# Kernel tuning notes

Measured on AMD Instinct MI355X. Metric: run time of the kernel, lower is better.

## Reference

```python
import jax, jax.numpy as jnp
import numpy as np
from jax import lax

B, C, H, W = 8, 128, 128, 128
HEADS = 16
HEAD_C = C // HEADS  # 8
SLOPE = 0.2
EPS = 1e-12


def _conv(x, w, b, padding, groups=1):
    # x: [B,C,H,W], w: [O,I/groups,kh,kw]
    y = lax.conv_general_dilated(
        x, w, window_strides=(1, 1), padding=padding,
        dimension_numbers=("NCHW", "OIHW", "NCHW"),
        feature_group_count=groups)
    return y + b[None, :, None, None]


def _conv_block(x, conv1_w, conv1_b, conv2_w, conv2_b, dw_w, dw_b, sc_w, sc_b):
    h = _conv(x, conv1_w, conv1_b, ((1, 1), (1, 1)))            # 3x3, zero pad
    h = jnp.where(h >= 0, h, SLOPE * h)                          # LeakyReLU
    h = _conv(h, conv2_w, conv2_b, ((0, 0), (0, 0)))             # 1x1
    hp = jnp.pad(h, ((0, 0), (0, 0), (1, 1), (1, 1)), mode="reflect")
    h = _conv(hp, dw_w, dw_b, ((0, 0), (0, 0)), groups=C)        # depthwise 3x3, reflect pad
    h = jnp.where(h >= 0, h, SLOPE * h)
    sc = _conv(x, sc_w, sc_b, ((0, 0), (0, 0)))                  # 1x1 shortcut
    return h + sc


def setup_inputs() -> dict:
    key = jax.random.key(0)
    ks = jax.random.split(key, 10)
    s = 0.05
    return {
        "x1": jax.random.normal(ks[0], (B, C, H, W), jnp.float32),
        "x2": jax.random.normal(ks[1], (B, C, H, W), jnp.float32),
        "temperature": jnp.ones((HEADS, 1, 1), jnp.float32),
        "conv1_w": jax.random.normal(ks[2], (C, C, 3, 3), jnp.float32) * s,
        "conv1_b": jnp.zeros((C,), jnp.float32),
        "conv2_w": jax.random.normal(ks[3], (C, C, 1, 1), jnp.float32) * s,
        "conv2_b": jnp.zeros((C,), jnp.float32),
        "dw_w": jax.random.normal(ks[4], (C, 1, 3, 3), jnp.float32) * s,
        "dw_b": jnp.zeros((C,), jnp.float32),
        "sc_w": jax.random.normal(ks[5], (C, C, 1, 1), jnp.float32) * s,
        "sc_b": jnp.zeros((C,), jnp.float32),
    }


def reference(x1, x2, temperature, conv1_w, conv1_b, conv2_w, conv2_b,
              dw_w, dw_b, sc_w, sc_b):
    b, c, h, w = x2.shape
    # b (head c) h w -> b head c (h w)
    qk = x1.reshape(b, HEADS, HEAD_C, h * w)
    v = x2.reshape(b, HEADS, HEAD_C, h * w)
    # L2-normalize over spatial dim (F.normalize, eps=1e-12)
    norm = jnp.sqrt(jnp.sum(qk * qk, axis=-1, keepdims=True))
    qn = qk / jnp.maximum(norm, EPS)
    # channel attention: [b, head, c, c]
    attn = jnp.einsum("bhcn,bhdn->bhcd", qn, qn) * temperature
    attn = jax.nn.softmax(attn, axis=-1)
    out = jnp.einsum("bhcd,bhdn->bhcn", attn, v)
    out = out.reshape(b, c, h, w)
    out = _conv_block(out, conv1_w, conv1_b, conv2_w, conv2_b,
                      dw_w, dw_b, sc_w, sc_b)
    return out + x1
```

## Files before the change

### kernel.cpp

```cpp
#include <hip/hip_runtime.h>
#include <hip/hip_bf16.h>

typedef __attribute__((ext_vector_type(8))) short short8;
typedef __attribute__((ext_vector_type(4))) float f32x4;

#define NB 8
#define NC 128
#define NHW 128
#define NSP (NHW*NHW)
#define SLOPE 0.2f
#define EPSN 1e-12f

static __device__ __forceinline__ unsigned short f2bf(float f) {
    __hip_bfloat16 h = __float2bfloat16(f);
    return *reinterpret_cast<unsigned short*>(&h);
}
static __device__ __forceinline__ float bf2f(__hip_bfloat16 h) {
    return __bfloat162float(h);
}

__global__ void prep_wb1(const float* __restrict__ w, __hip_bfloat16* __restrict__ wb) {
    int idx = blockIdx.x * 256 + threadIdx.x;
    if (idx >= 128 * 128 * 9) return;
    int kw = idx % 3; int t = idx / 3;
    int kh = t % 3;   t /= 3;
    int i  = t % 128; int o = t / 128;
    int tap = kh * 3 + kw;
    int q = i >> 5, lk = (i >> 3) & 3, j = i & 7;
    int wn = o >> 6, c = (o >> 4) & 3, l15 = o & 15;
    int lane = lk * 16 + l15;
    size_t chunk = ((size_t)(tap * 4 + q) * 2 + wn) * 4 + c;
    wb[chunk * 512 + lane * 8 + j] = __float2bfloat16(w[idx]);
}

__global__ void prep_w1x1(const float* __restrict__ w, __hip_bfloat16* __restrict__ wb) {
    int idx = blockIdx.x * 256 + threadIdx.x;
    if (idx >= 128 * 128) return;
    int i = idx & 127, o = idx >> 7;
    int kk = i >> 5, lk = (i >> 3) & 3, j = i & 7;
    int wn = o >> 6, c = (o >> 4) & 3, l15 = o & 15;
    int lane = lk * 16 + l15;
    size_t chunk = ((size_t)(wn * 4 + kk) * 4 + c);
    wb[chunk * 512 + lane * 8 + j] = __float2bfloat16(w[idx]);
}

__global__ __launch_bounds__(256) void gram_part(const float* __restrict__ x1,
                                                 float* __restrict__ Gp) {
    int bh = blockIdx.x & 127;
    int q  = blockIdx.x >> 7;
    const float* base = x1 + (size_t)bh * 8 * NSP + q * 4096;
    float acc[8][8];
#pragma unroll
    for (int c = 0; c < 8; c++)
#pragma unroll
        for (int d = 0; d < 8; d++) acc[c][d] = 0.f;

    for (int n = threadIdx.x; n < 4096; n += 256) {
        float v[8];
#pragma unroll
        for (int c = 0; c < 8; c++) v[c] = base[c * NSP + n];
#pragma unroll
        for (int c = 0; c < 8; c++)
#pragma unroll
            for (int d = 0; d < 8; d++)
                acc[c][d] = fmaf(v[c], v[d], acc[c][d]);
    }
#pragma unroll
    for (int c = 0; c < 8; c++)
#pragma unroll
        for (int d = 0; d < 8; d++)
            for (int off = 32; off > 0; off >>= 1)
                acc[c][d] += __shfl_down(acc[c][d], off);

    __shared__ float red[4][64];
    int wv = threadIdx.x >> 6;
    if ((threadIdx.x & 63) == 0) {
#pragma unroll
        for (int c = 0; c < 8; c++)
#pragma unroll
            for (int d = 0; d < 8; d++) red[wv][c * 8 + d] = acc[c][d];
    }
    __syncthreads();
    if (threadIdx.x < 64)
        Gp[(size_t)(q * 128 + bh) * 64 + threadIdx.x] =
            red[0][threadIdx.x] + red[1][threadIdx.x] + red[2][threadIdx.x] + red[3][threadIdx.x];
}

__global__ void gram_reduce(const float* __restrict__ Gp, float* __restrict__ G) {
    int bh = blockIdx.x;
    int t = threadIdx.x;
    float s = 0.f;
#pragma unroll
    for (int q = 0; q < 4; q++) s += Gp[(size_t)(q * 128 + bh) * 64 + t];
    G[bh * 64 + t] = s;
}

__global__ void softmax_kernel(const float* __restrict__ G, const float* __restrict__ temp,
                               float* __restrict__ attn) {
    int bh = blockIdx.x; int h = bh & 15;
    int t = threadIdx.x;
    int c = t >> 3, d = t & 7;
    const float* g = G + bh * 64;
    float nc = fmaxf(sqrtf(g[c * 8 + c]), EPSN);
    float nd = fmaxf(sqrtf(g[d * 8 + d]), EPSN);
    float a = g[t] / (nc * nd) * temp[h];
    float m = a;
#pragma unroll
    for (int off = 4; off > 0; off >>= 1) m = fmaxf(m, __shfl_xor(m, off));
    float e = __expf(a - m);
    float s = e;
#pragma unroll
    for (int off = 4; off > 0; off >>= 1) s += __shfl_xor(s, off);
    attn[bh * 64 + t] = e / s;
}

__global__ __launch_bounds__(256) void av_v2(const float* __restrict__ x2,
                                             const float* __restrict__ attn,
                                             __hip_bfloat16* __restrict__ yt) {
    int b  = blockIdx.x >> 8;
    int p0 = (blockIdx.x & 255) << 6;
    __shared__ float vt[128][65];
    __shared__ float at[16][65];
    for (int idx = threadIdx.x; idx < 1024; idx += 256)
        at[idx >> 6][idx & 63] = attn[(size_t)b * 1024 + idx];
    for (int idx = threadIdx.x; idx < 8192; idx += 256) {
        int row = idx >> 6, col = idx & 63;
        vt[row][col] = x2[(size_t)(b * 128 + row) * NSP + p0 + col];
    }
    __syncthreads();
    for (int idx = threadIdx.x; idx < 1024; idx += 256) {
        int cq = idx & 15;
        int p  = idx >> 4;
        float vv[8];
#pragma unroll
        for (int d = 0; d < 8; d++) vv[d] = vt[cq * 8 + d][p];
        unsigned int pk[4];
#pragma unroll
        for (int c = 0; c < 8; c += 2) {
            float s0 = 0.f, s1 = 0.f;
#pragma unroll
            for (int d = 0; d < 8; d++) {
                s0 = fmaf(at[cq][c * 8 + d], vv[d], s0);
                s1 = fmaf(at[cq][(c + 1) * 8 + d], vv[d], s1);
            }
            pk[c >> 1] = (unsigned int)f2bf(s0) | ((unsigned int)f2bf(s1) << 16);
        }
        uint4 st; st.x = pk[0]; st.y = pk[1]; st.z = pk[2]; st.w = pk[3];
        *reinterpret_cast<uint4*>(yt + ((size_t)b * NSP + p0 + p) * 128 + cq * 8) = st;
    }
}

__global__ __launch_bounds__(256, 3) void fused_conv(const __hip_bfloat16* __restrict__ yt,
                                                     const __hip_bfloat16* __restrict__ wb1,
                                                     const __hip_bfloat16* __restrict__ wb2,
                                                     const __hip_bfloat16* __restrict__ wbsc,
                                                     const float* __restrict__ b1,
                                                     const float* __restrict__ b2,
                                                     const float* __restrict__ bsc,
                                                     const float* __restrict__ x1,
                                                     __hip_bfloat16* __restrict__ h2,
                                                     float* __restrict__ out) {
    __shared__ uint4 smem[2048];
    char* smem_raw = (char*)smem;
    int bid = blockIdx.x;
    int blk = (bid & 7) * 128 + (bid >> 3);
    int b = blk >> 7, h = blk & 127;
    int tid = threadIdx.x;
    int lane = tid & 63;
    int wid = tid >> 6;
    int wm = wid >> 1, wn = wid & 1;
    int l15 = lane & 15;
    int lk = lane >> 4;

    const short8* wf1  = reinterpret_cast<const short8*>(wb1);
    const short8* wf2  = reinterpret_cast<const short8*>(wb2);
    const short8* wfsc = reinterpret_cast<const short8*>(wbsc);

    f32x4 acc[4][4];
#pragma unroll
    for (int a = 0; a < 4; a++)
#pragma unroll
        for (int c = 0; c < 4; c++) acc[a][c] = (f32x4){0.f, 0.f, 0.f, 0.f};

#pragma unroll
    for (int q = 0; q < 4; ++q) {
        __syncthreads();
        for (int idx = tid; idx < 1584; idx += 256) {
            int g = idx & 3;
            int colr = idx >> 2;
            int col = colr % 132;
            int r = colr / 132;
            int hh = h + r - 1;
            int w = col - 1;
            uint4 v = make_uint4(0u, 0u, 0u, 0u);
            if ((unsigned)hh < 128u && (unsigned)w < 128u)
                v = *reinterpret_cast<const uint4*>(
                    yt + (((size_t)(b * 128 + hh)) * 128 + w) * 128 + q * 32 + g * 8);
            smem[(r * 4 + g) * 132 + col] = v;
        }
        __syncthreads();

        const short8* wp0 = wf1 + ((size_t)((0 * 4 + q) * 2 + wn) * 4) * 64 + lane;
        short8 cb0 = wp0[0], cb1 = wp0[64], cb2 = wp0[128], cb3 = wp0[192];

#pragma unroll
        for (int tap = 0; tap < 9; ++tap) {
            int kh = tap / 3, kw = tap - kh * 3;
            short8 nb0, nb1, nb2, nb3;
            if (tap < 8) {
                const short8* wpn = wf1 + ((size_t)(((tap + 1) * 4 + q) * 2 + wn) * 4) * 64 + lane;
                nb0 = wpn[0]; nb1 = wpn[64]; nb2 = wpn[128]; nb3 = wpn[192];
            }
            short8 afr[4];
#pragma unroll
            for (int a = 0; a < 4; ++a) {
                int col = (wm * 4 + a) * 16 + l15 + kw;
                afr[a] = *reinterpret_cast<const short8*>(&smem[(kh * 4 + lk) * 132 + col]);
            }
            __builtin_amdgcn_s_setprio(1);
#pragma unroll
            for (int a = 0; a < 4; ++a) {
                acc[a][0] = __builtin_amdgcn_mfma_f32_16x16x32_bf16(afr[a], cb0, acc[a][0], 0, 0, 0);
                acc[a][1] = __builtin_amdgcn_mfma_f32_16x16x32_bf16(afr[a], cb1, acc[a][1], 0, 0, 0);
                acc[a][2] = __builtin_amdgcn_mfma_f32_16x16x32_bf16(afr[a], cb2, acc[a][2], 0, 0, 0);
                acc[a][3] = __builtin_amdgcn_mfma_f32_16x16x32_bf16(afr[a], cb3, acc[a][3], 0, 0, 0);
            }
            __builtin_amdgcn_s_setprio(0);
            if (tap < 8) { cb0 = nb0; cb1 = nb1; cb2 = nb2; cb3 = nb3; }
        }
    }

    __syncthreads();
#pragma unroll
    for (int c = 0; c < 4; ++c) {
        int o = wn * 64 + c * 16 + l15;
        float bv = b1[o];
        int go = o >> 3, ob = (o & 7) << 1;
#pragma unroll
        for (int a = 0; a < 4; ++a) {
            int pb = (wm * 4 + a) * 16 + lk * 4;
#pragma unroll
            for (int j = 0; j < 4; ++j) {
                int p = pb + j;
                float v = acc[a][c][j] + bv;
                v = v >= 0.f ? v : SLOPE * v;
                *reinterpret_cast<__hip_bfloat16*>(
                    smem_raw + p * 256 + (((go ^ (p & 15)) << 4) | ob)) = __float2bfloat16(v);
            }
        }
    }
    __syncthreads();

#pragma unroll
    for (int a = 0; a < 4; a++)
#pragma unroll
        for (int c = 0; c < 4; c++) acc[a][c] = (f32x4){0.f, 0.f, 0.f, 0.f};
#pragma unroll
    for (int kk = 0; kk < 4; ++kk) {
        short8 bfr[4];
#pragma unroll
        for (int c = 0; c < 4; ++c)
            bfr[c] = wf2[((size_t)(wn * 4 + kk) * 4 + c) * 64 + lane];
        short8 afr[4];
        int g = kk * 4 + lk;
#pragma unroll
        for (int a = 0; a < 4; ++a) {
            int p = (wm * 4 + a) * 16 + l15;
            afr[a] = *reinterpret_cast<const short8*>(smem_raw + p * 256 + ((g ^ (p & 15)) << 4));
        }
        __builtin_amdgcn_s_setprio(1);
#pragma unroll
        for (int a = 0; a < 4; ++a)
#pragma unroll
            for (int c = 0; c < 4; ++c)
                acc[a][c] = __builtin_amdgcn_mfma_f32_16x16x32_bf16(afr[a], bfr[c], acc[a][c], 0, 0, 0);
        __builtin_amdgcn_s_setprio(0);
    }
#pragma unroll
    for (int c = 0; c < 4; ++c) {
        int o = wn * 64 + c * 16 + l15;
        float bv = b2[o];
        size_t obase = ((size_t)(b * 128 + o) * 128 + h) * 128;
#pragma unroll
        for (int a = 0; a < 4; ++a) {
            int w0 = (wm * 4 + a) * 16 + lk * 4;
            uint2 st;
            st.x = (unsigned int)f2bf(acc[a][c][0] + bv) | ((unsigned int)f2bf(acc[a][c][1] + bv) << 16);
            st.y = (unsigned int)f2bf(acc[a][c][2] + bv) | ((unsigned int)f2bf(acc[a][c][3] + bv) << 16);
            *reinterpret_cast<uint2*>(h2 + obase + w0) = st;
        }
    }

    __syncthreads();
    for (int idx = tid; idx < 2048; idx += 256) {
        int p = idx >> 4, g = idx & 15;
        uint4 v = *reinterpret_cast<const uint4*>(
            yt + ((size_t)(b * NSP + h * 128 + p)) * 128 + g * 8);
        *reinterpret_cast<uint4*>(smem_raw + p * 256 + ((g ^ (p & 15)) << 4)) = v;
    }
    __syncthreads();

#pragma unroll
    for (int a = 0; a < 4; a++)
#pragma unroll
        for (int c = 0; c < 4; c++) acc[a][c] = (f32x4){0.f, 0.f, 0.f, 0.f};
#pragma unroll
    for (int kk = 0; kk < 4; ++kk) {
        short8 bfr[4];
#pragma unroll
        for (int c = 0; c < 4; ++c)
            bfr[c] = wfsc[((size_t)(wn * 4 + kk) * 4 + c) * 64 + lane];
        short8 afr[4];
        int g = kk * 4 + lk;
#pragma unroll
        for (int a = 0; a < 4; ++a) {
            int p = (wm * 4 + a) * 16 + l15;
            afr[a] = *reinterpret_cast<const short8*>(smem_raw + p * 256 + ((g ^ (p & 15)) << 4));
        }
        __builtin_amdgcn_s_setprio(1);
#pragma unroll
        for (int a = 0; a < 4; ++a)
#pragma unroll
            for (int c = 0; c < 4; ++c)
                acc[a][c] = __builtin_amdgcn_mfma_f32_16x16x32_bf16(afr[a], bfr[c], acc[a][c], 0, 0, 0);
        __builtin_amdgcn_s_setprio(0);
    }
#pragma unroll
    for (int c = 0; c < 4; ++c) {
        int o = wn * 64 + c * 16 + l15;
        float bv = bsc[o];
        size_t obase = ((size_t)(b * 128 + o) * 128 + h) * 128;
#pragma unroll
        for (int a = 0; a < 4; ++a) {
            int w0 = (wm * 4 + a) * 16 + lk * 4;
            float4 xv = *reinterpret_cast<const float4*>(x1 + obase + w0);
            float4 st;
            st.x = acc[a][c][0] + bv + xv.x;
            st.y = acc[a][c][1] + bv + xv.y;
            st.z = acc[a][c][2] + bv + xv.z;
            st.w = acc[a][c][3] + bv + xv.w;
            *reinterpret_cast<float4*>(out + obase + w0) = st;
        }
    }
}

__global__ __launch_bounds__(256) void dw_v2(const __hip_bfloat16* __restrict__ h2,
                                             const float* __restrict__ dww,
                                             const float* __restrict__ dwb,
                                             float* __restrict__ out) {
    int bid = blockIdx.x;
    int swz = (bid & 7) * 1024 + (bid >> 3);
    size_t tidx = (size_t)swz * 256 + threadIdx.x;
    int w0 = (int)((tidx & 15) << 3);
    int hh = (int)((tidx >> 4) & 127);
    int bc = (int)(tidx >> 11);
    int c  = bc & 127;
    const __hip_bfloat16* src = h2 + ((size_t)bc << 14);
    float wg[9];
#pragma unroll
    for (int k = 0; k < 9; ++k) wg[k] = dww[c * 9 + k];
    float bv = dwb[c];
    float a8[8];
#pragma unroll
    for (int j = 0; j < 8; ++j) a8[j] = bv;
#pragma unroll
    for (int kh = 0; kh < 3; ++kh) {
        int ih = hh + kh - 1;
        ih = ih < 0 ? 1 : (ih > 127 ? 126 : ih);
        const __hip_bfloat16* row = src + ih * 128;
        short8 mid = *reinterpret_cast<const short8*>(row + w0);
        float v[10];
        v[0] = bf2f(row[w0 == 0 ? 1 : w0 - 1]);
#pragma unroll
        for (int j = 0; j < 8; ++j)
            v[j + 1] = __uint_as_float((unsigned int)(unsigned short)mid[j] << 16);
        v[9] = bf2f(row[w0 == 120 ? 126 : w0 + 8]);
#pragma unroll
        for (int kw = 0; kw < 3; ++kw)
#pragma unroll
            for (int j = 0; j < 8; ++j)
                a8[j] = fmaf(v[j + kw], wg[kh * 3 + kw], a8[j]);
    }
    size_t ob = ((size_t)bc << 14) + hh * 128 + w0;
    float4 o0 = *reinterpret_cast<const float4*>(out + ob);
    float4 o1 = *reinterpret_cast<const float4*>(out + ob + 4);
#pragma unroll
    for (int j = 0; j < 8; ++j) a8[j] = a8[j] >= 0.f ? a8[j] : SLOPE * a8[j];
    o0.x += a8[0]; o0.y += a8[1]; o0.z += a8[2]; o0.w += a8[3];
    o1.x += a8[4]; o1.y += a8[5]; o1.z += a8[6]; o1.w += a8[7];
    *reinterpret_cast<float4*>(out + ob) = o0;
    *reinterpret_cast<float4*>(out + ob + 4) = o1;
}

extern "C" void kernel_launch(void* const* d_in, const int* in_sizes, int n_in,
                              void* d_out, int out_size, void* d_ws, size_t ws_size,
                              hipStream_t stream) {
    const float* x1   = (const float*)d_in[0];
    const float* x2   = (const float*)d_in[1];
    const float* temp = (const float*)d_in[2];
    const float* c1w  = (const float*)d_in[3];
    const float* c1b  = (const float*)d_in[4];
    const float* c2w  = (const float*)d_in[5];
    const float* c2b  = (const float*)d_in[6];
    const float* dww  = (const float*)d_in[7];
    const float* dwb  = (const float*)d_in[8];
    const float* scw  = (const float*)d_in[9];
    const float* scb  = (const float*)d_in[10];
    float* out = (float*)d_out;
    char* ws = (char*)d_ws;

    float*          G    = (float*)(ws);
    float*          attn = (float*)(ws + (32 << 10));
    float*          Gp   = (float*)(ws + (64 << 10));
    __hip_bfloat16* wb1  = (__hip_bfloat16*)(ws + (192 << 10));
    __hip_bfloat16* wb2  = (__hip_bfloat16*)(ws + (480 << 10));
    __hip_bfloat16* wbsc = (__hip_bfloat16*)(ws + (512 << 10));
    __hip_bfloat16* yt   = (__hip_bfloat16*)(ws + ((size_t)1 << 20));
    __hip_bfloat16* h2b  = (__hip_bfloat16*)(ws + ((size_t)34 << 20));

    prep_wb1<<<576, 256, 0, stream>>>(c1w, wb1);
    prep_w1x1<<<64, 256, 0, stream>>>(c2w, wb2);
    prep_w1x1<<<64, 256, 0, stream>>>(scw, wbsc);

    gram_part<<<512, 256, 0, stream>>>(x1, Gp);
    gram_reduce<<<128, 64, 0, stream>>>(Gp, G);
    softmax_kernel<<<128, 64, 0, stream>>>(G, temp, attn);
    av_v2<<<2048, 256, 0, stream>>>(x2, attn, yt);

    fused_conv<<<1024, 256, 0, stream>>>(yt, wb1, wb2, wbsc, c1b, c2b, scb, x1, h2b, out);
    dw_v2<<<8192, 256, 0, stream>>>(h2b, dww, dwb, out);
}
```

Before: 159.8 us.

## Split fused conv tiles to half rows with 64-channel K stages and swizzled LDS

The fused conv block now processes half an image row (64 pixels) per workgroup instead of a full row, which doubles the grid to 2048 blocks and halves the accumulators. The input halo is staged in two 64-channel halves with an XOR-swizzled LDS layout, and the 3x3 weights are re-laid out so each stage walks 18 tap/sub-chunk steps. Shared memory drops from 32 KB to about 25 KB and the occupancy hint rises to 4 blocks per CU, aiming for better latency hiding and load balance. In exchange the halo overhead grows (66 of 64 columns), and weight fragments are reloaded twice as often per output pixel.

```diff
diff --git a/kernel.cpp b/kernel.cpp
--- a/kernel.cpp
+++ b/kernel.cpp
@@ -26,10 +26,10 @@
     int kh = t % 3;   t /= 3;
     int i  = t % 128; int o = t / 128;
     int tap = kh * 3 + kw;
-    int q = i >> 5, lk = (i >> 3) & 3, j = i & 7;
+    int half = i >> 6, icc = (i >> 5) & 1, lk = (i >> 3) & 3, j = i & 7;
     int wn = o >> 6, c = (o >> 4) & 3, l15 = o & 15;
     int lane = lk * 16 + l15;
-    size_t chunk = ((size_t)(tap * 4 + q) * 2 + wn) * 4 + c;
+    size_t chunk = (size_t)tap * 32 + half * 16 + wn * 8 + icc * 4 + c;
     wb[chunk * 512 + lane * 8 + j] = __float2bfloat16(w[idx]);
 }
 
@@ -150,7 +150,7 @@
     }
 }
 
-__global__ __launch_bounds__(256, 3) void fused_conv(const __hip_bfloat16* __restrict__ yt,
+__global__ __launch_bounds__(256, 4) void fused_conv(const __hip_bfloat16* __restrict__ yt,
                                                      const __hip_bfloat16* __restrict__ wb1,
                                                      const __hip_bfloat16* __restrict__ wb2,
                                                      const __hip_bfloat16* __restrict__ wbsc,
@@ -160,11 +160,14 @@
                                                      const float* __restrict__ x1,
                                                      __hip_bfloat16* __restrict__ h2,
                                                      float* __restrict__ out) {
-    __shared__ uint4 smem[2048];
+    __shared__ uint4 smem[1584];
     char* smem_raw = (char*)smem;
     int bid = blockIdx.x;
-    int blk = (bid & 7) * 128 + (bid >> 3);
-    int b = blk >> 7, h = blk & 127;
+    int swz = (bid & 7) * 256 + (bid >> 3);
+    int b = swz >> 8;
+    int rh = swz & 255;
+    int h = rh >> 1;
+    int p0 = (rh & 1) * 64;
     int tid = threadIdx.x;
     int lane = tid & 63;
     int wid = tid >> 6;
@@ -176,57 +179,63 @@
     const short8* wf2  = reinterpret_cast<const short8*>(wb2);
     const short8* wfsc = reinterpret_cast<const short8*>(wbsc);
 
-    f32x4 acc[4][4];
-#pragma unroll
-    for (int a = 0; a < 4; a++)
+    f32x4 acc[2][4];
+#pragma unroll
+    for (int a = 0; a < 2; a++)
 #pragma unroll
         for (int c = 0; c < 4; c++) acc[a][c] = (f32x4){0.f, 0.f, 0.f, 0.f};
 
 #pragma unroll
-    for (int q = 0; q < 4; ++q) {
+    for (int half = 0; half < 2; ++half) {
         __syncthreads();
         for (int idx = tid; idx < 1584; idx += 256) {
-            int g = idx & 3;
-            int colr = idx >> 2;
-            int col = colr % 132;
-            int r = colr / 132;
+            int g = idx & 7;
+            int colr = idx >> 3;
+            int col = colr % 66;
+            int r = colr / 66;
             int hh = h + r - 1;
-            int w = col - 1;
+            int w = p0 + col - 1;
             uint4 v = make_uint4(0u, 0u, 0u, 0u);
             if ((unsigned)hh < 128u && (unsigned)w < 128u)
                 v = *reinterpret_cast<const uint4*>(
-                    yt + (((size_t)(b * 128 + hh)) * 128 + w) * 128 + q * 32 + g * 8);
-            smem[(r * 4 + g) * 132 + col] = v;
+                    yt + (((size_t)(b * 128 + hh)) * 128 + w) * 128 + half * 64 + g * 8);
+            smem[(r * 66 + col) * 8 + (g ^ (col & 7))] = v;
         }
         __syncthreads();
 
-        const short8* wp0 = wf1 + ((size_t)((0 * 4 + q) * 2 + wn) * 4) * 64 + lane;
+        int cgrp = half * 16 + wn * 8;
+        const short8* wp0 = wf1 + (size_t)cgrp * 64 + lane;
         short8 cb0 = wp0[0], cb1 = wp0[64], cb2 = wp0[128], cb3 = wp0[192];
 
 #pragma unroll
-        for (int tap = 0; tap < 9; ++tap) {
+        for (int gi = 0; gi < 18; ++gi) {
+            int tap = gi >> 1, icc = gi & 1;
             int kh = tap / 3, kw = tap - kh * 3;
             short8 nb0, nb1, nb2, nb3;
-            if (tap < 8) {
-                const short8* wpn = wf1 + ((size_t)(((tap + 1) * 4 + q) * 2 + wn) * 4) * 64 + lane;
+            if (gi < 17) {
+                int gin = gi + 1;
+                const short8* wpn = wf1 +
+                    (size_t)(((gin >> 1) * 32) + cgrp + (gin & 1) * 4) * 64 + lane;
                 nb0 = wpn[0]; nb1 = wpn[64]; nb2 = wpn[128]; nb3 = wpn[192];
             }
-            short8 afr[4];
-#pragma unroll
-            for (int a = 0; a < 4; ++a) {
-                int col = (wm * 4 + a) * 16 + l15 + kw;
-                afr[a] = *reinterpret_cast<const short8*>(&smem[(kh * 4 + lk) * 132 + col]);
+            short8 afr[2];
+#pragma unroll
+            for (int a = 0; a < 2; ++a) {
+                int col = (wm * 2 + a) * 16 + l15 + kw;
+                int g = icc * 4 + lk;
+                afr[a] = *reinterpret_cast<const short8*>(
+                    &smem[(kh * 66 + col) * 8 + (g ^ (col & 7))]);
             }
             __builtin_amdgcn_s_setprio(1);
 #pragma unroll
-            for (int a = 0; a < 4; ++a) {
+            for (int a = 0; a < 2; ++a) {
                 acc[a][0] = __builtin_amdgcn_mfma_f32_16x16x32_bf16(afr[a], cb0, acc[a][0], 0, 0, 0);
                 acc[a][1] = __builtin_amdgcn_mfma_f32_16x16x32_bf16(afr[a], cb1, acc[a][1], 0, 0, 0);
                 acc[a][2] = __builtin_amdgcn_mfma_f32_16x16x32_bf16(afr[a], cb2, acc[a][2], 0, 0, 0);
                 acc[a][3] = __builtin_amdgcn_mfma_f32_16x16x32_bf16(afr[a], cb3, acc[a][3], 0, 0, 0);
             }
             __builtin_amdgcn_s_setprio(0);
-            if (tap < 8) { cb0 = nb0; cb1 = nb1; cb2 = nb2; cb3 = nb3; }
+            cb0 = nb0; cb1 = nb1; cb2 = nb2; cb3 = nb3;
         }
     }
 
@@ -237,8 +246,8 @@
         float bv = b1[o];
         int go = o >> 3, ob = (o & 7) << 1;
 #pragma unroll
-        for (int a = 0; a < 4; ++a) {
-            int pb = (wm * 4 + a) * 16 + lk * 4;
+        for (int a = 0; a < 2; ++a) {
+            int pb = (wm * 2 + a) * 16 + lk * 4;
 #pragma unroll
             for (int j = 0; j < 4; ++j) {
                 int p = pb + j;
@@ -252,7 +261,7 @@
     __syncthreads();
 
 #pragma unroll
-    for (int a = 0; a < 4; a++)
+    for (int a = 0; a < 2; a++)
 #pragma unroll
         for (int c = 0; c < 4; c++) acc[a][c] = (f32x4){0.f, 0.f, 0.f, 0.f};
 #pragma unroll
@@ -261,16 +270,16 @@
 #pragma unroll
         for (int c = 0; c < 4; ++c)
             bfr[c] = wf2[((size_t)(wn * 4 + kk) * 4 + c) * 64 + lane];
-        short8 afr[4];
+        short8 afr[2];
         int g = kk * 4 + lk;
 #pragma unroll
-        for (int a = 0; a < 4; ++a) {
-            int p = (wm * 4 + a) * 16 + l15;
+        for (int a = 0; a < 2; ++a) {
+            int p = (wm * 2 + a) * 16 + l15;
             afr[a] = *reinterpret_cast<const short8*>(smem_raw + p * 256 + ((g ^ (p & 15)) << 4));
         }
         __builtin_amdgcn_s_setprio(1);
 #pragma unroll
-        for (int a = 0; a < 4; ++a)
+        for (int a = 0; a < 2; ++a)
 #pragma unroll
             for (int c = 0; c < 4; ++c)
                 acc[a][c] = __builtin_amdgcn_mfma_f32_16x16x32_bf16(afr[a], bfr[c], acc[a][c], 0, 0, 0);
@@ -280,10 +289,10 @@
     for (int c = 0; c < 4; ++c) {
         int o = wn * 64 + c * 16 + l15;
         float bv = b2[o];
-        size_t obase = ((size_t)(b * 128 + o) * 128 + h) * 128;
-#pragma unroll
-        for (int a = 0; a < 4; ++a) {
-            int w0 = (wm * 4 + a) * 16 + lk * 4;
+        size_t obase = ((size_t)(b * 128 + o) * 128 + h) * 128 + p0;
+#pragma unroll
+        for (int a = 0; a < 2; ++a) {
+            int w0 = (wm * 2 + a) * 16 + lk * 4;
             uint2 st;
             st.x = (unsigned int)f2bf(acc[a][c][0] + bv) | ((unsigned int)f2bf(acc[a][c][1] + bv) << 16);
             st.y = (unsigned int)f2bf(acc[a][c][2] + bv) | ((unsigned int)f2bf(acc[a][c][3] + bv) << 16);
@@ -292,16 +301,16 @@
     }
 
     __syncthreads();
-    for (int idx = tid; idx < 2048; idx += 256) {
+    for (int idx = tid; idx < 1024; idx += 256) {
         int p = idx >> 4, g = idx & 15;
         uint4 v = *reinterpret_cast<const uint4*>(
-            yt + ((size_t)(b * NSP + h * 128 + p)) * 128 + g * 8);
+            yt + ((size_t)(b * NSP + h * 128 + p0 + p)) * 128 + g * 8);
         *reinterpret_cast<uint4*>(smem_raw + p * 256 + ((g ^ (p & 15)) << 4)) = v;
     }
     __syncthreads();
 
 #pragma unroll
-    for (int a = 0; a < 4; a++)
+    for (int a = 0; a < 2; a++)
 #pragma unroll
         for (int c = 0; c < 4; c++) acc[a][c] = (f32x4){0.f, 0.f, 0.f, 0.f};
 #pragma unroll
@@ -310,16 +319,16 @@
 #pragma unroll
         for (int c = 0; c < 4; ++c)
             bfr[c] = wfsc[((size_t)(wn * 4 + kk) * 4 + c) * 64 + lane];
-        short8 afr[4];
+        short8 afr[2];
         int g = kk * 4 + lk;
 #pragma unroll
-        for (int a = 0; a < 4; ++a) {
-            int p = (wm * 4 + a) * 16 + l15;
+        for (int a = 0; a < 2; ++a) {
+            int p = (wm * 2 + a) * 16 + l15;
             afr[a] = *reinterpret_cast<const short8*>(smem_raw + p * 256 + ((g ^ (p & 15)) << 4));
         }
         __builtin_amdgcn_s_setprio(1);
 #pragma unroll
-        for (int a = 0; a < 4; ++a)
+        for (int a = 0; a < 2; ++a)
 #pragma unroll
             for (int c = 0; c < 4; ++c)
                 acc[a][c] = __builtin_amdgcn_mfma_f32_16x16x32_bf16(afr[a], bfr[c], acc[a][c], 0, 0, 0);
@@ -329,10 +338,10 @@
     for (int c = 0; c < 4; ++c) {
         int o = wn * 64 + c * 16 + l15;
         float bv = bsc[o];
-        size_t obase = ((size_t)(b * 128 + o) * 128 + h) * 128;
-#pragma unroll
-        for (int a = 0; a < 4; ++a) {
-            int w0 = (wm * 4 + a) * 16 + lk * 4;
+        size_t obase = ((size_t)(b * 128 + o) * 128 + h) * 128 + p0;
+#pragma unroll
+        for (int a = 0; a < 2; ++a) {
+            int w0 = (wm * 2 + a) * 16 + lk * 4;
             float4 xv = *reinterpret_cast<const float4*>(x1 + obase + w0);
             float4 st;
             st.x = acc[a][c][0] + bv + xv.x;
@@ -427,6 +436,6 @@
     softmax_kernel<<<128, 64, 0, stream>>>(G, temp, attn);
     av_v2<<<2048, 256, 0, stream>>>(x2, attn, yt);
 
-    fused_conv<<<1024, 256, 0, stream>>>(yt, wb1, wb2, wbsc, c1b, c2b, scb, x1, h2b, out);
+    fused_conv<<<2048, 256, 0, stream>>>(yt, wb1, wb2, wbsc, c1b, c2b, scb, x1, h2b, out);
     dw_v2<<<8192, 256, 0, stream>>>(h2b, dww, dwb, out);
 }
```

Result: no change. 162.4 us (+1.6%).

## Pad activations in global memory and load conv A-fragments directly, halve tile

Applied to the files above, without the earlier changes.

The attention output is now written into a zero-bordered 130x130 NHWC buffer, with a small kernel zeroing the border, so the 3x3 conv can read its A fragments straight from global memory with no bounds checks and no LDS staging. Each block now covers half an image row (64 pixels) with each wave owning 32 output channels, which halves LDS use and doubles the block count. Launch bounds are raised to 5 blocks per SM. This removes the staging barriers and LDS traffic of the conv1 stage, but relies on L1/L2 for the overlapping reads across taps.

```diff
diff --git a/kernel.cpp b/kernel.cpp
--- a/kernel.cpp
+++ b/kernel.cpp
@@ -10,6 +10,7 @@
 #define NSP (NHW*NHW)
 #define SLOPE 0.2f
 #define EPSN 1e-12f
+#define PADW 130
 
 static __device__ __forceinline__ unsigned short f2bf(float f) {
     __hip_bfloat16 h = __float2bfloat16(f);
@@ -26,10 +27,10 @@
     int kh = t % 3;   t /= 3;
     int i  = t % 128; int o = t / 128;
     int tap = kh * 3 + kw;
-    int q = i >> 5, lk = (i >> 3) & 3, j = i & 7;
-    int wn = o >> 6, c = (o >> 4) & 3, l15 = o & 15;
+    int g32 = i >> 5, lk = (i >> 3) & 3, j = i & 7;
+    int f = o >> 4, l15 = o & 15;
     int lane = lk * 16 + l15;
-    size_t chunk = ((size_t)(tap * 4 + q) * 2 + wn) * 4 + c;
+    size_t chunk = (size_t)(tap * 4 + g32) * 8 + f;
     wb[chunk * 512 + lane * 8 + j] = __float2bfloat16(w[idx]);
 }
 
@@ -38,10 +39,25 @@
     if (idx >= 128 * 128) return;
     int i = idx & 127, o = idx >> 7;
     int kk = i >> 5, lk = (i >> 3) & 3, j = i & 7;
-    int wn = o >> 6, c = (o >> 4) & 3, l15 = o & 15;
+    int f = o >> 4, l15 = o & 15;
     int lane = lk * 16 + l15;
-    size_t chunk = ((size_t)(wn * 4 + kk) * 4 + c);
+    size_t chunk = (size_t)kk * 8 + f;
     wb[chunk * 512 + lane * 8 + j] = __float2bfloat16(w[idx]);
+}
+
+__global__ void pad_zero(__hip_bfloat16* __restrict__ yt2) {
+    int t = blockIdx.x * 256 + threadIdx.x;
+    if (t >= 8 * 516) return;
+    int b = t / 516, s = t % 516;
+    int row, col;
+    if (s < 130)      { row = 0;           col = s; }
+    else if (s < 260) { row = 129;         col = s - 130; }
+    else if (s < 388) { row = s - 260 + 1; col = 0; }
+    else              { row = s - 388 + 1; col = 129; }
+    uint4* dst = reinterpret_cast<uint4*>(yt2 + ((size_t)(b * PADW + row) * PADW + col) * 128);
+    uint4 z = make_uint4(0u, 0u, 0u, 0u);
+#pragma unroll
+    for (int i = 0; i < 16; ++i) dst[i] = z;
 }
 
 __global__ __launch_bounds__(256) void gram_part(const float* __restrict__ x1,
@@ -114,9 +130,9 @@
     attn[bh * 64 + t] = e / s;
 }
 
-__global__ __launch_bounds__(256) void av_v2(const float* __restrict__ x2,
+__global__ __launch_bounds__(256) void av_v3(const float* __restrict__ x2,
                                              const float* __restrict__ attn,
-                                             __hip_bfloat16* __restrict__ yt) {
+                                             __hip_bfloat16* __restrict__ yt2) {
     int b  = blockIdx.x >> 8;
     int p0 = (blockIdx.x & 255) << 6;
     __shared__ float vt[128][65];
@@ -146,11 +162,14 @@
             pk[c >> 1] = (unsigned int)f2bf(s0) | ((unsigned int)f2bf(s1) << 16);
         }
         uint4 st; st.x = pk[0]; st.y = pk[1]; st.z = pk[2]; st.w = pk[3];
-        *reinterpret_cast<uint4*>(yt + ((size_t)b * NSP + p0 + p) * 128 + cq * 8) = st;
-    }
-}
-
-__global__ __launch_bounds__(256, 3) void fused_conv(const __hip_bfloat16* __restrict__ yt,
+        int n = p0 + p;
+        int hh = n >> 7, wc = n & 127;
+        *reinterpret_cast<uint4*>(
+            yt2 + ((size_t)(b * PADW + hh + 1) * PADW + wc + 1) * 128 + cq * 8) = st;
+    }
+}
+
+__global__ __launch_bounds__(256, 5) void fused_conv(const __hip_bfloat16* __restrict__ yt2,
                                                      const __hip_bfloat16* __restrict__ wb1,
                                                      const __hip_bfloat16* __restrict__ wb2,
                                                      const __hip_bfloat16* __restrict__ wbsc,
@@ -160,15 +179,17 @@
                                                      const float* __restrict__ x1,
                                                      __hip_bfloat16* __restrict__ h2,
                                                      float* __restrict__ out) {
-    __shared__ uint4 smem[2048];
+    __shared__ uint4 smem[1024];
     char* smem_raw = (char*)smem;
     int bid = blockIdx.x;
-    int blk = (bid & 7) * 128 + (bid >> 3);
-    int b = blk >> 7, h = blk & 127;
+    int swz = (bid & 7) * 256 + (bid >> 3);
+    int b = swz >> 8;
+    int rh = swz & 255;
+    int h = rh >> 1;
+    int p0 = (rh & 1) * 64;
     int tid = threadIdx.x;
     int lane = tid & 63;
     int wid = tid >> 6;
-    int wm = wid >> 1, wn = wid & 1;
     int l15 = lane & 15;
     int lk = lane >> 4;
 
@@ -176,73 +197,55 @@
     const short8* wf2  = reinterpret_cast<const short8*>(wb2);
     const short8* wfsc = reinterpret_cast<const short8*>(wbsc);
 
-    f32x4 acc[4][4];
-#pragma unroll
-    for (int a = 0; a < 4; a++)
-#pragma unroll
-        for (int c = 0; c < 4; c++) acc[a][c] = (f32x4){0.f, 0.f, 0.f, 0.f};
-
-#pragma unroll
-    for (int q = 0; q < 4; ++q) {
-        __syncthreads();
-        for (int idx = tid; idx < 1584; idx += 256) {
-            int g = idx & 3;
-            int colr = idx >> 2;
-            int col = colr % 132;
-            int r = colr / 132;
-            int hh = h + r - 1;
-            int w = col - 1;
-            uint4 v = make_uint4(0u, 0u, 0u, 0u);
-            if ((unsigned)hh < 128u && (unsigned)w < 128u)
-                v = *reinterpret_cast<const uint4*>(
-                    yt + (((size_t)(b * 128 + hh)) * 128 + w) * 128 + q * 32 + g * 8);
-            smem[(r * 4 + g) * 132 + col] = v;
-        }
-        __syncthreads();
-
-        const short8* wp0 = wf1 + ((size_t)((0 * 4 + q) * 2 + wn) * 4) * 64 + lane;
-        short8 cb0 = wp0[0], cb1 = wp0[64], cb2 = wp0[128], cb3 = wp0[192];
-
+    f32x4 acc[4][2];
+#pragma unroll
+    for (int m = 0; m < 4; m++) { acc[m][0] = (f32x4){0,0,0,0}; acc[m][1] = (f32x4){0,0,0,0}; }
+
+    const __hip_bfloat16* abase = yt2 + ((size_t)(b * PADW + h) * PADW + (p0 + l15)) * 128 + lk * 8;
+
+#pragma unroll
+    for (int g32 = 0; g32 < 4; ++g32) {
+        const short8* wp0 = wf1 + ((size_t)(0 * 4 + g32) * 8 + wid * 2) * 64 + lane;
+        short8 cb0 = wp0[0], cb1 = wp0[64];
 #pragma unroll
         for (int tap = 0; tap < 9; ++tap) {
             int kh = tap / 3, kw = tap - kh * 3;
-            short8 nb0, nb1, nb2, nb3;
+            short8 nb0, nb1;
             if (tap < 8) {
-                const short8* wpn = wf1 + ((size_t)(((tap + 1) * 4 + q) * 2 + wn) * 4) * 64 + lane;
-                nb0 = wpn[0]; nb1 = wpn[64]; nb2 = wpn[128]; nb3 = wpn[192];
+                const short8* wpn = wf1 + ((size_t)((tap + 1) * 4 + g32) * 8 + wid * 2) * 64 + lane;
+                nb0 = wpn[0]; nb1 = wpn[64];
             }
-            short8 afr[4];
-#pragma unroll
-            for (int a = 0; a < 4; ++a) {
-                int col = (wm * 4 + a) * 16 + l15 + kw;
-                afr[a] = *reinterpret_cast<const short8*>(&smem[(kh * 4 + lk) * 132 + col]);
-            }
+            const __hip_bfloat16* arow = abase + (size_t)(kh * PADW + kw) * 128 + g32 * 32;
+            short8 a0 = *reinterpret_cast<const short8*>(arow);
+            short8 a1 = *reinterpret_cast<const short8*>(arow + 2048);
+            short8 a2 = *reinterpret_cast<const short8*>(arow + 4096);
+            short8 a3 = *reinterpret_cast<const short8*>(arow + 6144);
             __builtin_amdgcn_s_setprio(1);
-#pragma unroll
-            for (int a = 0; a < 4; ++a) {
-                acc[a][0] = __builtin_amdgcn_mfma_f32_16x16x32_bf16(afr[a], cb0, acc[a][0], 0, 0, 0);
-                acc[a][1] = __builtin_amdgcn_mfma_f32_16x16x32_bf16(afr[a], cb1, acc[a][1], 0, 0, 0);
-                acc[a][2] = __builtin_amdgcn_mfma_f32_16x16x32_bf16(afr[a], cb2, acc[a][2], 0, 0, 0);
-                acc[a][3] = __builtin_amdgcn_mfma_f32_16x16x32_bf16(afr[a], cb3, acc[a][3], 0, 0, 0);
-            }
+            acc[0][0] = __builtin_amdgcn_mfma_f32_16x16x32_bf16(a0, cb0, acc[0][0], 0, 0, 0);
+            acc[0][1] = __builtin_amdgcn_mfma_f32_16x16x32_bf16(a0, cb1, acc[0][1], 0, 0, 0);
+            acc[1][0] = __builtin_amdgcn_mfma_f32_16x16x32_bf16(a1, cb0, acc[1][0], 0, 0, 0);
+            acc[1][1] = __builtin_amdgcn_mfma_f32_16x16x32_bf16(a1, cb1, acc[1][1], 0, 0, 0);
+            acc[2][0] = __builtin_amdgcn_mfma_f32_16x16x32_bf16(a2, cb0, acc[2][0], 0, 0, 0);
+            acc[2][1] = __builtin_amdgcn_mfma_f32_16x16x32_bf16(a2, cb1, acc[2][1], 0, 0, 0);
+            acc[3][0] = __builtin_amdgcn_mfma_f32_16x16x32_bf16(a3, cb0, acc[3][0], 0, 0, 0);
+            acc[3][1] = __builtin_amdgcn_mfma_f32_16x16x32_bf16(a3, cb1, acc[3][1], 0, 0, 0);
             __builtin_amdgcn_s_setprio(0);
-            if (tap < 8) { cb0 = nb0; cb1 = nb1; cb2 = nb2; cb3 = nb3; }
-        }
-    }
-
-    __syncthreads();
-#pragma unroll
-    for (int c = 0; c < 4; ++c) {
-        int o = wn * 64 + c * 16 + l15;
+            cb0 = nb0; cb1 = nb1;
+        }
+    }
+
+#pragma unroll
+    for (int c = 0; c < 2; ++c) {
+        int o = wid * 32 + c * 16 + l15;
         float bv = b1[o];
         int go = o >> 3, ob = (o & 7) << 1;
 #pragma unroll
-        for (int a = 0; a < 4; ++a) {
-            int pb = (wm * 4 + a) * 16 + lk * 4;
+        for (int m = 0; m < 4; ++m) {
+            int pb = m * 16 + lk * 4;
 #pragma unroll
             for (int j = 0; j < 4; ++j) {
                 int p = pb + j;
-                float v = acc[a][c][j] + bv;
+                float v = acc[m][c][j] + bv;
                 v = v >= 0.f ? v : SLOPE * v;
                 *reinterpret_cast<__hip_bfloat16*>(
                     smem_raw + p * 256 + (((go ^ (p & 15)) << 4) | ob)) = __float2bfloat16(v);
@@ -252,93 +255,85 @@
     __syncthreads();
 
 #pragma unroll
-    for (int a = 0; a < 4; a++)
-#pragma unroll
-        for (int c = 0; c < 4; c++) acc[a][c] = (f32x4){0.f, 0.f, 0.f, 0.f};
+    for (int m = 0; m < 4; m++) { acc[m][0] = (f32x4){0,0,0,0}; acc[m][1] = (f32x4){0,0,0,0}; }
 #pragma unroll
     for (int kk = 0; kk < 4; ++kk) {
-        short8 bfr[4];
-#pragma unroll
-        for (int c = 0; c < 4; ++c)
-            bfr[c] = wf2[((size_t)(wn * 4 + kk) * 4 + c) * 64 + lane];
+        short8 bf0 = wf2[((size_t)kk * 8 + wid * 2 + 0) * 64 + lane];
+        short8 bf1 = wf2[((size_t)kk * 8 + wid * 2 + 1) * 64 + lane];
         short8 afr[4];
         int g = kk * 4 + lk;
 #pragma unroll
-        for (int a = 0; a < 4; ++a) {
-            int p = (wm * 4 + a) * 16 + l15;
-            afr[a] = *reinterpret_cast<const short8*>(smem_raw + p * 256 + ((g ^ (p & 15)) << 4));
+        for (int m = 0; m < 4; ++m) {
+            int p = m * 16 + l15;
+            afr[m] = *reinterpret_cast<const short8*>(smem_raw + p * 256 + ((g ^ (p & 15)) << 4));
         }
         __builtin_amdgcn_s_setprio(1);
 #pragma unroll
-        for (int a = 0; a < 4; ++a)
-#pragma unroll
-            for (int c = 0; c < 4; ++c)
-                acc[a][c] = __builtin_amdgcn_mfma_f32_16x16x32_bf16(afr[a], bfr[c], acc[a][c], 0, 0, 0);
+        for (int m = 0; m < 4; ++m) {
+            acc[m][0] = __builtin_amdgcn_mfma_f32_16x16x32_bf16(afr[m], bf0, acc[m][0], 0, 0, 0);
+            acc[m][1] = __builtin_amdgcn_mfma_f32_16x16x32_bf16(afr[m], bf1, acc[m][1], 0, 0, 0);
+        }
         __builtin_amdgcn_s_setprio(0);
     }
 #pragma unroll
-    for (int c = 0; c < 4; ++c) {
-        int o = wn * 64 + c * 16 + l15;
+    for (int c = 0; c < 2; ++c) {
+        int o = wid * 32 + c * 16 + l15;
         float bv = b2[o];
-        size_t obase = ((size_t)(b * 128 + o) * 128 + h) * 128;
-#pragma unroll
-        for (int a = 0; a < 4; ++a) {
-            int w0 = (wm * 4 + a) * 16 + lk * 4;
+        size_t obase = ((size_t)(b * 128 + o) * 128 + h) * 128 + p0;
+#pragma unroll
+        for (int m = 0; m < 4; ++m) {
+            int w0 = m * 16 + lk * 4;
             uint2 st;
-            st.x = (unsigned int)f2bf(acc[a][c][0] + bv) | ((unsigned int)f2bf(acc[a][c][1] + bv) << 16);
-            st.y = (unsigned int)f2bf(acc[a][c][2] + bv) | ((unsigned int)f2bf(acc[a][c][3] + bv) << 16);
+            st.x = (unsigned int)f2bf(acc[m][c][0] + bv) | ((unsigned int)f2bf(acc[m][c][1] + bv) << 16);
+            st.y = (unsigned int)f2bf(acc[m][c][2] + bv) | ((unsigned int)f2bf(acc[m][c][3] + bv) << 16);
             *reinterpret_cast<uint2*>(h2 + obase + w0) = st;
         }
     }
 
     __syncthreads();
-    for (int idx = tid; idx < 2048; idx += 256) {
+    for (int idx = tid; idx < 1024; idx += 256) {
         int p = idx >> 4, g = idx & 15;
         uint4 v = *reinterpret_cast<const uint4*>(
-            yt + ((size_t)(b * NSP + h * 128 + p)) * 128 + g * 8);
+            yt2 + ((size_t)(b * PADW + h + 1) * PADW + (p0 + 1 + p)) * 128 + g * 8);
         *reinterpret_cast<uint4*>(smem_raw + p * 256 + ((g ^ (p & 15)) << 4)) = v;
     }
     __syncthreads();
 
 #pragma unroll
-    for (int a = 0; a < 4; a++)
-#pragma unroll
-        for (int c = 0; c < 4; c++) acc[a][c] = (f32x4){0.f, 0.f, 0.f, 0.f};
+    for (int m = 0; m < 4; m++) { acc[m][0] = (f32x4){0,0,0,0}; acc[m][1] = (f32x4){0,0,0,0}; }
 #pragma unroll
     for (int kk = 0; kk < 4; ++kk) {
-        short8 bfr[4];
-#pragma unroll
-        for (int c = 0; c < 4; ++c)
-            bfr[c] = wfsc[((size_t)(wn * 4 + kk) * 4 + c) * 64 + lane];
+        short8 bf0 = wfsc[((size_t)kk * 8 + wid * 2 + 0) * 64 + lane];
+        short8 bf1 = wfsc[((size_t)kk * 8 + wid * 2 + 1) * 64 + lane];
         short8 afr[4];
         int g = kk * 4 + lk;
 #pragma unroll
-        for (int a = 0; a < 4; ++a) {
-            int p = (wm * 4 + a) * 16 + l15;
-            afr[a] = *reinterpret_cast<const short8*>(smem_raw + p * 256 + ((g ^ (p & 15)) << 4));
+        for (int m = 0; m < 4; ++m) {
+            int p = m * 16 + l15;
+            afr[m] = *reinterpret_cast<const short8*>(smem_raw + p * 256 + ((g ^ (p & 15)) << 4));
         }
         __builtin_amdgcn_s_setprio(1);
 #pragma unroll
-        for (int a = 0; a < 4; ++a)
-#pragma unroll
-            for (int c = 0; c < 4; ++c)
-                acc[a][c] = __builtin_amdgcn_mfma_f32_16x16x32_bf16(afr[a], bfr[c], acc[a][c], 0, 0, 0);
+        for (int m = 0; m < 4; ++m) {
+            acc[m][0] = __builtin_amdgcn_mfma_f32_16x16x32_bf16(afr[m], bf0, acc[m][0], 0, 0, 0);
+            acc[m][1] = __builtin_amdgcn_mfma_f32_16x16x32_bf16(afr[m], bf1, acc[m][1], 0, 0, 0);
+        }
         __builtin_amdgcn_s_setprio(0);
     }
 #pragma unroll
-    for (int c = 0; c < 4; ++c) {
-        int o = wn * 64 + c * 16 + l15;
+    for (int c = 0; c < 2; ++c) {
+        int o = wid * 32 + c * 16 + l15;
         float bv = bsc[o];
-        size_t obase = ((size_t)(b * 128 + o) * 128 + h) * 128;
-#pragma unroll
-        for (int a = 0; a < 4; ++a) {
-            int w0 = (wm * 4 + a) * 16 + lk * 4;
+        size_t obase = ((size_t)(b * 128 + o) * 128 + h) * 128 + p0;
+#pragma unroll
+        for (int m = 0; m < 4; ++m) {
+            int w0 = m * 16 + lk * 4;
             float4 xv = *reinterpret_cast<const float4*>(x1 + obase + w0);
             float4 st;
-            st.x = acc[a][c][0] + bv + xv.x;
-            st.y = acc[a][c][1] + bv + xv.y;
-            st.z = acc[a][c][2] + bv + xv.z;
-            st.w = acc[a][c][3] + bv + xv.w;
+            st.x = acc[m][c][0] + bv + xv.x;
+            st.y = acc[m][c][1] + bv + xv.y;
+            st.z = acc[m][c][2] + bv + xv.z;
+            st.w = acc[m][c][3] + bv + xv.w;
             *reinterpret_cast<float4*>(out + obase + w0) = st;
         }
     }
@@ -415,18 +410,19 @@
     __hip_bfloat16* wb1  = (__hip_bfloat16*)(ws + (192 << 10));
     __hip_bfloat16* wb2  = (__hip_bfloat16*)(ws + (480 << 10));
     __hip_bfloat16* wbsc = (__hip_bfloat16*)(ws + (512 << 10));
-    __hip_bfloat16* yt   = (__hip_bfloat16*)(ws + ((size_t)1 << 20));
-    __hip_bfloat16* h2b  = (__hip_bfloat16*)(ws + ((size_t)34 << 20));
+    __hip_bfloat16* yt2  = (__hip_bfloat16*)(ws + ((size_t)1 << 20));
+    __hip_bfloat16* h2b  = (__hip_bfloat16*)(ws + ((size_t)36 << 20));
 
     prep_wb1<<<576, 256, 0, stream>>>(c1w, wb1);
     prep_w1x1<<<64, 256, 0, stream>>>(c2w, wb2);
     prep_w1x1<<<64, 256, 0, stream>>>(scw, wbsc);
+    pad_zero<<<17, 256, 0, stream>>>(yt2);
 
     gram_part<<<512, 256, 0, stream>>>(x1, Gp);
     gram_reduce<<<128, 64, 0, stream>>>(Gp, G);
     softmax_kernel<<<128, 64, 0, stream>>>(G, temp, attn);
-    av_v2<<<2048, 256, 0, stream>>>(x2, attn, yt);
-
-    fused_conv<<<1024, 256, 0, stream>>>(yt, wb1, wb2, wbsc, c1b, c2b, scb, x1, h2b, out);
+    av_v3<<<2048, 256, 0, stream>>>(x2, attn, yt2);
+
+    fused_conv<<<2048, 256, 0, stream>>>(yt2, wb1, wb2, wbsc, c1b, c2b, scb, x1, h2b, out);
     dw_v2<<<8192, 256, 0, stream>>>(h2b, dww, dwb, out);
 }
```

After: 261.7 us. 1.64x slower.

## Pre-pad conv input buffer and stream 3x3 weights into LDS via async loads

Applied to the files above, without the earlier changes.

The attention output is now written into a zero-padded 130x130 NHWC buffer, so the 3x3 conv staging loop drops its bounds checks. Conv1 weights are double-buffered in LDS with global_load_lds async copies instead of register prefetch. The activation tile in LDS gets an XOR swizzle to reduce bank conflicts. The cost is a larger LDS footprint (about 41 KB per block), an extra __syncthreads per tap, an extra border-zeroing kernel, and reworked weight layouts for all three weight sets.

```diff
diff --git a/kernel.cpp b/kernel.cpp
--- a/kernel.cpp
+++ b/kernel.cpp
@@ -10,6 +10,7 @@
 #define NSP (NHW*NHW)
 #define SLOPE 0.2f
 #define EPSN 1e-12f
+#define PADW 130
 
 static __device__ __forceinline__ unsigned short f2bf(float f) {
     __hip_bfloat16 h = __float2bfloat16(f);
@@ -17,6 +18,11 @@
 }
 static __device__ __forceinline__ float bf2f(__hip_bfloat16 h) {
     return __bfloat162float(h);
+}
+static __device__ __forceinline__ void gld16(const void* g, void* l) {
+    __builtin_amdgcn_global_load_lds(
+        (const __attribute__((address_space(1))) void*)g,
+        (__attribute__((address_space(3))) void*)l, 16, 0, 0);
 }
 
 __global__ void prep_wb1(const float* __restrict__ w, __hip_bfloat16* __restrict__ wb) {
@@ -27,9 +33,9 @@
     int i  = t % 128; int o = t / 128;
     int tap = kh * 3 + kw;
     int q = i >> 5, lk = (i >> 3) & 3, j = i & 7;
-    int wn = o >> 6, c = (o >> 4) & 3, l15 = o & 15;
+    int f = o >> 4, l15 = o & 15;
     int lane = lk * 16 + l15;
-    size_t chunk = ((size_t)(tap * 4 + q) * 2 + wn) * 4 + c;
+    size_t chunk = (size_t)(tap * 4 + q) * 8 + f;
     wb[chunk * 512 + lane * 8 + j] = __float2bfloat16(w[idx]);
 }
 
@@ -38,10 +44,25 @@
     if (idx >= 128 * 128) return;
     int i = idx & 127, o = idx >> 7;
     int kk = i >> 5, lk = (i >> 3) & 3, j = i & 7;
-    int wn = o >> 6, c = (o >> 4) & 3, l15 = o & 15;
+    int f = o >> 4, l15 = o & 15;
     int lane = lk * 16 + l15;
-    size_t chunk = ((size_t)(wn * 4 + kk) * 4 + c);
+    size_t chunk = (size_t)kk * 8 + f;
     wb[chunk * 512 + lane * 8 + j] = __float2bfloat16(w[idx]);
+}
+
+__global__ void pad_zero(__hip_bfloat16* __restrict__ yt2) {
+    int t = blockIdx.x * 256 + threadIdx.x;
+    if (t >= 8 * 516) return;
+    int b = t / 516, s = t % 516;
+    int row, col;
+    if (s < 130)      { row = 0;           col = s; }
+    else if (s < 260) { row = 129;         col = s - 130; }
+    else if (s < 388) { row = s - 260 + 1; col = 0; }
+    else              { row = s - 388 + 1; col = 129; }
+    uint4* dst = reinterpret_cast<uint4*>(yt2 + ((size_t)(b * PADW + row) * PADW + col) * 128);
+    uint4 z = make_uint4(0u, 0u, 0u, 0u);
+#pragma unroll
+    for (int i = 0; i < 16; ++i) dst[i] = z;
 }
 
 __global__ __launch_bounds__(256) void gram_part(const float* __restrict__ x1,
@@ -114,9 +135,9 @@
     attn[bh * 64 + t] = e / s;
 }
 
-__global__ __launch_bounds__(256) void av_v2(const float* __restrict__ x2,
+__global__ __launch_bounds__(256) void av_v3(const float* __restrict__ x2,
                                              const float* __restrict__ attn,
-                                             __hip_bfloat16* __restrict__ yt) {
+                                             __hip_bfloat16* __restrict__ yt2) {
     int b  = blockIdx.x >> 8;
     int p0 = (blockIdx.x & 255) << 6;
     __shared__ float vt[128][65];
@@ -146,11 +167,14 @@
             pk[c >> 1] = (unsigned int)f2bf(s0) | ((unsigned int)f2bf(s1) << 16);
         }
         uint4 st; st.x = pk[0]; st.y = pk[1]; st.z = pk[2]; st.w = pk[3];
-        *reinterpret_cast<uint4*>(yt + ((size_t)b * NSP + p0 + p) * 128 + cq * 8) = st;
-    }
-}
-
-__global__ __launch_bounds__(256, 3) void fused_conv(const __hip_bfloat16* __restrict__ yt,
+        int n = p0 + p;
+        int hh = n >> 7, wc = n & 127;
+        *reinterpret_cast<uint4*>(
+            yt2 + ((size_t)(b * PADW + hh + 1) * PADW + wc + 1) * 128 + cq * 8) = st;
+    }
+}
+
+__global__ __launch_bounds__(256, 3) void fused_conv(const __hip_bfloat16* __restrict__ yt2,
                                                      const __hip_bfloat16* __restrict__ wb1,
                                                      const __hip_bfloat16* __restrict__ wb2,
                                                      const __hip_bfloat16* __restrict__ wbsc,
@@ -160,7 +184,7 @@
                                                      const float* __restrict__ x1,
                                                      __hip_bfloat16* __restrict__ h2,
                                                      float* __restrict__ out) {
-    __shared__ uint4 smem[2048];
+    __shared__ uint4 smem[2584];
     char* smem_raw = (char*)smem;
     int bid = blockIdx.x;
     int blk = (bid & 7) * 128 + (bid >> 3);
@@ -172,7 +196,6 @@
     int l15 = lane & 15;
     int lk = lane >> 4;
 
-    const short8* wf1  = reinterpret_cast<const short8*>(wb1);
     const short8* wf2  = reinterpret_cast<const short8*>(wb2);
     const short8* wfsc = reinterpret_cast<const short8*>(wbsc);
 
@@ -182,55 +205,69 @@
 #pragma unroll
         for (int c = 0; c < 4; c++) acc[a][c] = (f32x4){0.f, 0.f, 0.f, 0.f};
 
-#pragma unroll
-    for (int q = 0; q < 4; ++q) {
+    {
+        const char* gsrc = (const char*)wb1 + (size_t)(wid * 64 + lane) * 16;
+        int lb = __builtin_amdgcn_readfirstlane(24960 + wid * 1024);
+        gld16(gsrc, smem_raw + lb);
+        gld16(gsrc + 4096, smem_raw + lb + 4096);
+    }
+
+#pragma unroll
+    for (int q2 = 0; q2 < 4; ++q2) {
         __syncthreads();
-        for (int idx = tid; idx < 1584; idx += 256) {
-            int g = idx & 3;
+        for (int idx = tid; idx < 1560; idx += 256) {
+            int gr = idx & 3;
             int colr = idx >> 2;
-            int col = colr % 132;
-            int r = colr / 132;
-            int hh = h + r - 1;
-            int w = col - 1;
-            uint4 v = make_uint4(0u, 0u, 0u, 0u);
-            if ((unsigned)hh < 128u && (unsigned)w < 128u)
-                v = *reinterpret_cast<const uint4*>(
-                    yt + (((size_t)(b * 128 + hh)) * 128 + w) * 128 + q * 32 + g * 8);
-            smem[(r * 4 + g) * 132 + col] = v;
+            int col = colr % 130;
+            int r = colr / 130;
+            uint4 v = *reinterpret_cast<const uint4*>(
+                yt2 + (((size_t)(b * PADW + h + r)) * PADW + col) * 128 + q2 * 32 + gr * 8);
+            int cp = col >> 1;
+            int g = (col & 1) * 4 + gr;
+            smem[(r * 65 + cp) * 8 + (g ^ (cp & 7))] = v;
         }
         __syncthreads();
 
-        const short8* wp0 = wf1 + ((size_t)((0 * 4 + q) * 2 + wn) * 4) * 64 + lane;
-        short8 cb0 = wp0[0], cb1 = wp0[64], cb2 = wp0[128], cb3 = wp0[192];
-
 #pragma unroll
         for (int tap = 0; tap < 9; ++tap) {
-            int kh = tap / 3, kw = tap - kh * 3;
-            short8 nb0, nb1, nb2, nb3;
-            if (tap < 8) {
-                const short8* wpn = wf1 + ((size_t)(((tap + 1) * 4 + q) * 2 + wn) * 4) * 64 + lane;
-                nb0 = wpn[0]; nb1 = wpn[64]; nb2 = wpn[128]; nb3 = wpn[192];
+            const int s = q2 * 9 + tap;
+            const int buf = s & 1;
+            if (s < 35) {
+                const int qn = (tap == 8) ? q2 + 1 : q2;
+                const int tn = (tap == 8) ? 0 : tap + 1;
+                const char* gsrc = (const char*)wb1 + (size_t)(tn * 4 + qn) * 8192
+                                   + (size_t)(wid * 64 + lane) * 16;
+                int lb = __builtin_amdgcn_readfirstlane(24960 + (buf ^ 1) * 8192 + wid * 1024);
+                gld16(gsrc, smem_raw + lb);
+                gld16(gsrc + 4096, smem_raw + lb + 4096);
             }
+            const int kh = tap / 3, kw = tap - (tap / 3) * 3;
             short8 afr[4];
 #pragma unroll
             for (int a = 0; a < 4; ++a) {
                 int col = (wm * 4 + a) * 16 + l15 + kw;
-                afr[a] = *reinterpret_cast<const short8*>(&smem[(kh * 4 + lk) * 132 + col]);
+                int cp = col >> 1;
+                int g = (col & 1) * 4 + lk;
+                afr[a] = *reinterpret_cast<const short8*>(&smem[(kh * 65 + cp) * 8 + (g ^ (cp & 7))]);
             }
+            const char* bb = smem_raw + 24960 + buf * 8192;
+            short8 bfr[4];
+#pragma unroll
+            for (int c = 0; c < 4; ++c)
+                bfr[c] = *reinterpret_cast<const short8*>(bb + ((wn * 4 + c) * 64 + lane) * 16);
             __builtin_amdgcn_s_setprio(1);
 #pragma unroll
             for (int a = 0; a < 4; ++a) {
-                acc[a][0] = __builtin_amdgcn_mfma_f32_16x16x32_bf16(afr[a], cb0, acc[a][0], 0, 0, 0);
-                acc[a][1] = __builtin_amdgcn_mfma_f32_16x16x32_bf16(afr[a], cb1, acc[a][1], 0, 0, 0);
-                acc[a][2] = __builtin_amdgcn_mfma_f32_16x16x32_bf16(afr[a], cb2, acc[a][2], 0, 0, 0);
-                acc[a][3] = __builtin_amdgcn_mfma_f32_16x16x32_bf16(afr[a], cb3, acc[a][3], 0, 0, 0);
+                acc[a][0] = __builtin_amdgcn_mfma_f32_16x16x32_bf16(afr[a], bfr[0], acc[a][0], 0, 0, 0);
+                acc[a][1] = __builtin_amdgcn_mfma_f32_16x16x32_bf16(afr[a], bfr[1], acc[a][1], 0, 0, 0);
+                acc[a][2] = __builtin_amdgcn_mfma_f32_16x16x32_bf16(afr[a], bfr[2], acc[a][2], 0, 0, 0);
+                acc[a][3] = __builtin_amdgcn_mfma_f32_16x16x32_bf16(afr[a], bfr[3], acc[a][3], 0, 0, 0);
             }
             __builtin_amdgcn_s_setprio(0);
-            if (tap < 8) { cb0 = nb0; cb1 = nb1; cb2 = nb2; cb3 = nb3; }
-        }
-    }
-
-    __syncthreads();
+            __syncthreads();
+        }
+    }
+
 #pragma unroll
     for (int c = 0; c < 4; ++c) {
         int o = wn * 64 + c * 16 + l15;
@@ -260,7 +297,7 @@
         short8 bfr[4];
 #pragma unroll
         for (int c = 0; c < 4; ++c)
-            bfr[c] = wf2[((size_t)(wn * 4 + kk) * 4 + c) * 64 + lane];
+            bfr[c] = wf2[((size_t)(kk * 8) + wn * 4 + c) * 64 + lane];
         short8 afr[4];
         int g = kk * 4 + lk;
 #pragma unroll
@@ -295,7 +332,7 @@
     for (int idx = tid; idx < 2048; idx += 256) {
         int p = idx >> 4, g = idx & 15;
         uint4 v = *reinterpret_cast<const uint4*>(
-            yt + ((size_t)(b * NSP + h * 128 + p)) * 128 + g * 8);
+            yt2 + ((size_t)(b * PADW + h + 1) * PADW + (p + 1)) * 128 + g * 8);
         *reinterpret_cast<uint4*>(smem_raw + p * 256 + ((g ^ (p & 15)) << 4)) = v;
     }
     __syncthreads();
@@ -309,7 +346,7 @@
         short8 bfr[4];
 #pragma unroll
         for (int c = 0; c < 4; ++c)
-            bfr[c] = wfsc[((size_t)(wn * 4 + kk) * 4 + c) * 64 + lane];
+            bfr[c] = wfsc[((size_t)(kk * 8) + wn * 4 + c) * 64 + lane];
         short8 afr[4];
         int g = kk * 4 + lk;
 #pragma unroll
@@ -415,18 +452,19 @@
     __hip_bfloat16* wb1  = (__hip_bfloat16*)(ws + (192 << 10));
     __hip_bfloat16* wb2  = (__hip_bfloat16*)(ws + (480 << 10));
     __hip_bfloat16* wbsc = (__hip_bfloat16*)(ws + (512 << 10));
-    __hip_bfloat16* yt   = (__hip_bfloat16*)(ws + ((size_t)1 << 20));
-    __hip_bfloat16* h2b  = (__hip_bfloat16*)(ws + ((size_t)34 << 20));
+    __hip_bfloat16* yt2  = (__hip_bfloat16*)(ws + ((size_t)1 << 20));
+    __hip_bfloat16* h2b  = (__hip_bfloat16*)(ws + ((size_t)36 << 20));
 
     prep_wb1<<<576, 256, 0, stream>>>(c1w, wb1);
     prep_w1x1<<<64, 256, 0, stream>>>(c2w, wb2);
     prep_w1x1<<<64, 256, 0, stream>>>(scw, wbsc);
+    pad_zero<<<17, 256, 0, stream>>>(yt2);
 
     gram_part<<<512, 256, 0, stream>>>(x1, Gp);
     gram_reduce<<<128, 64, 0, stream>>>(Gp, G);
     softmax_kernel<<<128, 64, 0, stream>>>(G, temp, attn);
-    av_v2<<<2048, 256, 0, stream>>>(x2, attn, yt);
-
-    fused_conv<<<1024, 256, 0, stream>>>(yt, wb1, wb2, wbsc, c1b, c2b, scb, x1, h2b, out);
+    av_v3<<<2048, 256, 0, stream>>>(x2, attn, yt2);
+
+    fused_conv<<<1024, 256, 0, stream>>>(yt2, wb1, wb2, wbsc, c1b, c2b, scb, x1, h2b, out);
     dw_v2<<<8192, 256, 0, stream>>>(h2b, dww, dwb, out);
 }
```

Measured after the change: 164.5 us. 1.03x slower.
